# Kernel optimization log

Hardware: AMD Instinct MI355X
Metric: run time of the kernel (lower is better)

The kernel has to match this reference:

```python
import jax, jax.numpy as jnp
import numpy as np

N_NODES = 50000
N_EDGES = 600000
D_IN, D_HID, D_OUT = 128, 128, 64
KEEP_PROB = 0.5  # TF2: dp = args.dropout used as rate; kept mask values clip to 1.0


def setup_inputs() -> dict:
    key = jax.random.key(0)
    k = jax.random.split(key, 6)
    x = jax.random.normal(k[0], (N_NODES, D_IN), dtype=jnp.float32)
    edge_row = jax.random.randint(k[1], (N_EDGES,), 0, N_NODES, dtype=jnp.int64)
    edge_col = jax.random.randint(k[2], (N_EDGES,), 0, N_NODES, dtype=jnp.int64)
    edge_vals = jnp.ones((N_EDGES,), dtype=jnp.float32)
    # tf.nn.dropout(ones)->clip(max=1)->bool is a Bernoulli(keep) edge mask
    edge_mask = jax.random.bernoulli(k[3], KEEP_PROB, (N_EDGES,))
    W0 = jax.random.normal(k[4], (D_IN, D_HID), dtype=jnp.float32) * 0.05
    W1 = jax.random.normal(k[5], (D_HID, D_OUT), dtype=jnp.float32) * 0.05
    return {"x": x, "edge_row": edge_row, "edge_col": edge_col,
            "edge_vals": edge_vals, "edge_mask": edge_mask, "W0": W0, "W1": W1}


def reference(x, edge_row, edge_col, edge_vals, edge_mask, W0, W1):
    N = x.shape[0]
    # drop edges by zeroing values (equivalent to boolean_mask compaction)
    ev = edge_vals * edge_mask.astype(edge_vals.dtype)
    loop = jnp.arange(N, dtype=edge_row.dtype)
    row = jnp.concatenate([edge_row, loop])            # + sparse identity
    col = jnp.concatenate([edge_col, loop])
    vals = jnp.concatenate([ev, jnp.ones((N,), ev.dtype)])
    # degree renormalization: D^{-1/2} (A+I) D^{-1/2}
    deg = jax.ops.segment_sum(vals, row, num_segments=N)
    d_inv_sqrt = jnp.clip(deg ** -0.5, 0.0, 10.0)
    nvals = vals * d_inv_sqrt[row] * d_inv_sqrt[col]

    def spmm(h):  # support @ h via gather-multiply-scatter
        return jax.ops.segment_sum(nvals[:, None] * h[col], row, num_segments=N)

    h = jax.nn.relu(spmm(x @ W0))
    out = spmm(h @ W1)  # last layer: identity activation
    return out
```

## Files before the change

### kernel.cpp

```cpp
#include <hip/hip_runtime.h>
#include <hip/hip_bf16.h>


#define BLK 256
#define PADW 32

typedef __attribute__((ext_vector_type(8))) short short8v;
typedef __attribute__((ext_vector_type(8))) unsigned short ushort8v;
typedef __attribute__((ext_vector_type(4))) unsigned short ushort4v;
typedef __attribute__((ext_vector_type(4))) float float4v;

__device__ inline unsigned short f2b(float f) {
    __hip_bfloat16 h = __float2bfloat16(f);
    return *reinterpret_cast<unsigned short*>(&h);
}
__device__ inline float b2f(unsigned short u) {
    unsigned int v = (unsigned int)u << 16;
    return *reinterpret_cast<float*>(&v);
}

__global__ __launch_bounds__(BLK) void prepK(const float* __restrict__ W0,
                                             const float* __restrict__ W1,
                                             unsigned short* __restrict__ W0T,
                                             unsigned short* __restrict__ W1T,
                                             int* __restrict__ counts, int n) {
    int i = blockIdx.x * BLK + threadIdx.x;
    if (i < n) counts[i] = 0;
    if (i < 128 * 128) {
        int c = i >> 7, k = i & 127;
        W0T[i] = f2b(W0[k * 128 + c]);
    } else if (i < 128 * 128 + 64 * 128) {
        int j = i - 128 * 128;
        int c = j >> 7, k = j & 127;
        W1T[j] = f2b(W1[k * 64 + c]);
    }
}

__global__ __launch_bounds__(BLK) void phase1K(const int* __restrict__ erow,
                                               const int* __restrict__ ecolin,
                                               const int* __restrict__ emask,
                                               int* __restrict__ counts,
                                               int* __restrict__ epack, int e,
                                               const float* __restrict__ X,
                                               const unsigned short* __restrict__ W0T,
                                               unsigned short* __restrict__ XW,
                                               int M, int nbE) {
    constexpr int NC = 128, NT = NC / 16;
    __shared__ __align__(16) unsigned short sB[NC * 128];
    int t = threadIdx.x;

    if ((int)blockIdx.x < nbE) {
        int base = blockIdx.x * (2 * BLK) + t;
#pragma unroll
        for (int u = 0; u < 2; u++) {
            int i = base + u * BLK;
            if (i < e && emask[i]) {
                int r = erow[i];
                int rank = atomicAdd(&counts[r], 1);
                if (rank < PADW) epack[(size_t)r * PADW + rank] = ecolin[i];
            }
        }
        return;
    }

    int row0 = (blockIdx.x - nbE) * 64;
    for (int ch = t; ch < NC * 16; ch += BLK) {
        int row = ch >> 4, c16 = ch & 15;
        int dst = row * 128 + ((c16 * 8) ^ ((row & 7) << 3));
        *(ushort8v*)&sB[dst] = *(const ushort8v*)&W0T[row * 128 + c16 * 8];
    }
    __syncthreads();

    int w = t >> 6, l = t & 63;
    int arow = row0 + w * 16 + (l & 15);
    int kgrp = l >> 4;
    int bcol = l & 15;
    bool aval = arow < M;
    const float* Arow = X + (size_t)(aval ? arow : 0) * 128;

    float4v acc[NT];
#pragma unroll
    for (int nt = 0; nt < NT; nt++) acc[nt] = {0.f, 0.f, 0.f, 0.f};
#pragma unroll
    for (int ks = 0; ks < 4; ks++) {
        int koff = ks * 32 + kgrp * 8;
        float4 a0 = make_float4(0.f, 0.f, 0.f, 0.f);
        float4 a1 = make_float4(0.f, 0.f, 0.f, 0.f);
        if (aval) {
            a0 = *(const float4*)&Arow[koff];
            a1 = *(const float4*)&Arow[koff + 4];
        }
        short8v av;
        av[0] = (short)f2b(a0.x); av[1] = (short)f2b(a0.y);
        av[2] = (short)f2b(a0.z); av[3] = (short)f2b(a0.w);
        av[4] = (short)f2b(a1.x); av[5] = (short)f2b(a1.y);
        av[6] = (short)f2b(a1.z); av[7] = (short)f2b(a1.w);
#pragma unroll
        for (int nt = 0; nt < NT; nt++) {
            int brow = nt * 16 + bcol;
            short8v bv = *(short8v*)&sB[brow * 128 + (koff ^ ((brow & 7) << 3))];
            acc[nt] = __builtin_amdgcn_mfma_f32_16x16x32_bf16(av, bv, acc[nt], 0, 0, 0);
        }
    }
    int crow0 = row0 + w * 16 + kgrp * 4;
#pragma unroll
    for (int nt = 0; nt < NT; nt++) {
#pragma unroll
        for (int j = 0; j < 4; j++) {
            int r = crow0 + j;
            if (r < M) XW[(size_t)r * NC + nt * 16 + bcol] = f2b(acc[nt][j]);
        }
    }
}

__global__ __launch_bounds__(BLK) void fuse1K(const unsigned short* __restrict__ XW,
                                              const int* __restrict__ counts,
                                              const int* __restrict__ epack,
                                              const unsigned short* __restrict__ W1T,
                                              unsigned short* __restrict__ HW1s, int n) {
    __shared__ __align__(16) unsigned short sA[32 * 128];
    __shared__ __align__(16) int2 sE[32 * PADW];
    __shared__ int sK[32];
    __shared__ float sD[32];
    int t = threadIdx.x;
    int row0 = blockIdx.x * 32;

    {
        const int* esrc = epack + (size_t)row0 * PADW;
        for (int q = t; q < 32 * PADW; q += BLK) {
            int c = esrc[q];
            c = ((unsigned)c < (unsigned)n) ? c : 0;
            float dc = fminf(rsqrtf(1.0f + (float)counts[c]), 10.0f);
            sE[q] = make_int2(c, __float_as_int(dc));
        }
    }
    if (t < 32) {
        int r = row0 + t;
        int cnt = (r < n) ? counts[r] : 0;
        sK[t] = min(cnt, PADW);
        sD[t] = (r < n) ? fminf(rsqrtf(1.0f + (float)cnt), 10.0f) : 0.f;
    }
    __syncthreads();

    int g = t >> 3, li = t & 7;
    int d0 = li * 16;
    {
        int lr = g;
        int r = row0 + lr;
        int k = sK[lr];
        float dis = sD[lr];
        float acc[16];
        if (r < n) {
            ushort8v s0 = *(const ushort8v*)&XW[(size_t)r * 128 + d0];
            ushort8v s1 = *(const ushort8v*)&XW[(size_t)r * 128 + d0 + 8];
#pragma unroll
            for (int q = 0; q < 8; q++) {
                acc[q] = dis * b2f(s0[q]);
                acc[8 + q] = dis * b2f(s1[q]);
            }
        } else {
#pragma unroll
            for (int q = 0; q < 16; q++) acc[q] = 0.f;
        }
        const int2* eL = &sE[lr * PADW];
        for (int i = 0; i < k; i += 4) {
            int i1 = i + 1 < k ? i + 1 : k - 1;
            int i2 = i + 2 < k ? i + 2 : k - 1;
            int i3 = i + 3 < k ? i + 3 : k - 1;
            int2 e0 = eL[i], e1 = eL[i1], e2 = eL[i2], e3 = eL[i3];
            float v0 = __int_as_float(e0.y);
            float v1 = (i + 1 < k) ? __int_as_float(e1.y) : 0.f;
            float v2 = (i + 2 < k) ? __int_as_float(e2.y) : 0.f;
            float v3 = (i + 3 < k) ? __int_as_float(e3.y) : 0.f;
            ushort8v ga0 = *(const ushort8v*)&XW[(size_t)e0.x * 128 + d0];
            ushort8v gb0 = *(const ushort8v*)&XW[(size_t)e0.x * 128 + d0 + 8];
            ushort8v ga1 = *(const ushort8v*)&XW[(size_t)e1.x * 128 + d0];
            ushort8v gb1 = *(const ushort8v*)&XW[(size_t)e1.x * 128 + d0 + 8];
            ushort8v ga2 = *(const ushort8v*)&XW[(size_t)e2.x * 128 + d0];
            ushort8v gb2 = *(const ushort8v*)&XW[(size_t)e2.x * 128 + d0 + 8];
            ushort8v ga3 = *(const ushort8v*)&XW[(size_t)e3.x * 128 + d0];
            ushort8v gb3 = *(const ushort8v*)&XW[(size_t)e3.x * 128 + d0 + 8];
#pragma unroll
            for (int q = 0; q < 8; q++) {
                acc[q]     += v0 * b2f(ga0[q]) + v1 * b2f(ga1[q])
                            + v2 * b2f(ga2[q]) + v3 * b2f(ga3[q]);
                acc[8 + q] += v0 * b2f(gb0[q]) + v1 * b2f(gb1[q])
                            + v2 * b2f(gb2[q]) + v3 * b2f(gb3[q]);
            }
        }
        ushort8v h0, h1;
#pragma unroll
        for (int q = 0; q < 8; q++) {
            h0[q] = f2b(fmaxf(acc[q], 0.f) * dis);
            h1[q] = f2b(fmaxf(acc[8 + q], 0.f) * dis);
        }
        int sw = (lr & 7) << 3;
        *(ushort8v*)&sA[lr * 128 + (d0 ^ sw)] = h0;
        *(ushort8v*)&sA[lr * 128 + ((d0 + 8) ^ sw)] = h1;
    }
    __syncthreads();

    int w = t >> 6, l = t & 63;
    int rt = w & 1, ct = w >> 1;
    int arow = rt * 16 + (l & 15);
    int kgrp = l >> 4;
    int bcol = l & 15;
    float4v acc2[2];
    acc2[0] = {0.f, 0.f, 0.f, 0.f};
    acc2[1] = {0.f, 0.f, 0.f, 0.f};
#pragma unroll
    for (int ks = 0; ks < 4; ks++) {
        int koff = ks * 32 + kgrp * 8;
        short8v av = *(short8v*)&sA[arow * 128 + (koff ^ ((arow & 7) << 3))];
#pragma unroll
        for (int nt = 0; nt < 2; nt++) {
            int brow = ct * 32 + nt * 16 + bcol;
            short8v bv = *(const short8v*)&W1T[brow * 128 + koff];
            acc2[nt] = __builtin_amdgcn_mfma_f32_16x16x32_bf16(av, bv, acc2[nt], 0, 0, 0);
        }
    }
    int lrow0 = rt * 16 + kgrp * 4;
#pragma unroll
    for (int nt = 0; nt < 2; nt++) {
#pragma unroll
        for (int j = 0; j < 4; j++) {
            int r = row0 + lrow0 + j;
            if (r < n)
                HW1s[(size_t)r * 64 + ct * 32 + nt * 16 + bcol] =
                    f2b(acc2[nt][j] * sD[lrow0 + j]);
        }
    }
}

__global__ __launch_bounds__(BLK) void spmm2K(const unsigned short* __restrict__ HW1s,
                                              const int* __restrict__ counts,
                                              const int* __restrict__ epack,
                                              float* __restrict__ out, int n) {
    int t = threadIdx.x;
    int r = blockIdx.x * 32 + (t >> 3);
    int li = t & 7;
    if (r >= n) return;
    int cnt = counts[r];
    int k = min(cnt, PADW);
    int d0 = li * 8;
    float acc[8];
    {
        ushort8v sv = *(const ushort8v*)&HW1s[(size_t)r * 64 + d0];
#pragma unroll
        for (int q = 0; q < 8; q++) acc[q] = b2f(sv[q]);
    }
    const int* eb = epack + (size_t)r * PADW;
    for (int i = 0; i < k; i += 8) {
        int cc[8];
        float vv[8];
#pragma unroll
        for (int j = 0; j < 8; j++) {
            int idx = (i + j < k) ? i + j : k - 1;
            cc[j] = eb[idx];
            vv[j] = (i + j < k) ? 1.f : 0.f;
        }
        ushort8v gg[8];
#pragma unroll
        for (int j = 0; j < 8; j++)
            gg[j] = *(const ushort8v*)&HW1s[(size_t)cc[j] * 64 + d0];
#pragma unroll
        for (int j = 0; j < 8; j++) {
#pragma unroll
            for (int q = 0; q < 8; q++) acc[q] += vv[j] * b2f(gg[j][q]);
        }
    }
    float dis = fminf(rsqrtf(1.0f + (float)cnt), 10.0f);
    float4 o0 = make_float4(acc[0] * dis, acc[1] * dis, acc[2] * dis, acc[3] * dis);
    float4 o1 = make_float4(acc[4] * dis, acc[5] * dis, acc[6] * dis, acc[7] * dis);
    *(float4*)&out[(size_t)r * 64 + d0] = o0;
    *(float4*)&out[(size_t)r * 64 + d0 + 4] = o1;
}


extern "C" void kernel_launch(void* const* d_in, const int* in_sizes, int n_in,
                              void* d_out, int out_size, void* d_ws, size_t ws_size,
                              hipStream_t stream) {
    const float* x = (const float*)d_in[0];
    const int* erow = (const int*)d_in[1];
    const int* ecolin = (const int*)d_in[2];
    const int* emask = (const int*)d_in[4];
    const float* W0 = (const float*)d_in[5];
    const float* W1 = (const float*)d_in[6];
    float* out = (float*)d_out;

    const int n = in_sizes[0] / 128;
    const int e = in_sizes[1];

    char* ws = (char*)d_ws;
    size_t off = 0;
    auto alloc = [&](size_t bytes) {
        void* p = ws + off;
        off += (bytes + 255) & ~(size_t)255;
        return p;
    };
    int* counts = (int*)alloc((size_t)n * 4);
    int* epack = (int*)alloc((size_t)n * PADW * 4);
    unsigned short* W0T = (unsigned short*)alloc(128 * 128 * 2);
    unsigned short* W1T = (unsigned short*)alloc(64 * 128 * 2);
    unsigned short* XW = (unsigned short*)alloc((size_t)n * 128 * 2);
    unsigned short* HW1s = (unsigned short*)alloc((size_t)n * 64 * 2);

    int nbP = (n + BLK - 1) / BLK;
    int nbE = (e + 2 * BLK - 1) / (2 * BLK);
    int nbG = (n + 63) / 64;
    int nbF = (n + 31) / 32;
    int nbS = (n + 31) / 32;

    prepK<<<nbP, BLK, 0, stream>>>(W0, W1, W0T, W1T, counts, n);
    phase1K<<<nbE + nbG, BLK, 0, stream>>>(erow, ecolin, emask,
                                           counts, epack, e,
                                           x, W0T, XW, n, nbE);
    fuse1K<<<nbF, BLK, 0, stream>>>(XW, counts, epack, W1T, HW1s, n);
    spmm2K<<<nbS, BLK, 0, stream>>>(HW1s, counts, epack, out, n);
}
```

Before: 69.39 us.

## Fold weight prep into phase1 kernel and replace count zeroing with memset

Removes the separate prep kernel. Each GEMM block now converts and transposes W0 from fp32 directly into shared memory, W1 transposition runs in extra tail blocks of phase1, and the counts buffer is cleared with hipMemsetAsync. GEMM blocks now process two 64-row tiles each so the per-block W0 staging is amortized, and edge blocks handle four edges per thread. The aim is to drop one kernel launch and its serialization. The cost is redundant W0 conversion in every GEMM block, scalar strided shared-memory stores, and fewer blocks for the GEMM.

```diff
diff --git a/kernel.cpp b/kernel.cpp
--- a/kernel.cpp
+++ b/kernel.cpp
@@ -17,23 +17,6 @@
 __device__ inline float b2f(unsigned short u) {
     unsigned int v = (unsigned int)u << 16;
     return *reinterpret_cast<float*>(&v);
-}
-
-__global__ __launch_bounds__(BLK) void prepK(const float* __restrict__ W0,
-                                             const float* __restrict__ W1,
-                                             unsigned short* __restrict__ W0T,
-                                             unsigned short* __restrict__ W1T,
-                                             int* __restrict__ counts, int n) {
-    int i = blockIdx.x * BLK + threadIdx.x;
-    if (i < n) counts[i] = 0;
-    if (i < 128 * 128) {
-        int c = i >> 7, k = i & 127;
-        W0T[i] = f2b(W0[k * 128 + c]);
-    } else if (i < 128 * 128 + 64 * 128) {
-        int j = i - 128 * 128;
-        int c = j >> 7, k = j & 127;
-        W1T[j] = f2b(W1[k * 64 + c]);
-    }
 }
 
 __global__ __launch_bounds__(BLK) void phase1K(const int* __restrict__ erow,
@@ -42,17 +25,20 @@
                                                int* __restrict__ counts,
                                                int* __restrict__ epack, int e,
                                                const float* __restrict__ X,
-                                               const unsigned short* __restrict__ W0T,
+                                               const float* __restrict__ W0,
+                                               const float* __restrict__ W1,
+                                               unsigned short* __restrict__ W1T,
                                                unsigned short* __restrict__ XW,
-                                               int M, int nbE) {
+                                               int M, int nbE, int nbG) {
     constexpr int NC = 128, NT = NC / 16;
     __shared__ __align__(16) unsigned short sB[NC * 128];
     int t = threadIdx.x;
-
-    if ((int)blockIdx.x < nbE) {
-        int base = blockIdx.x * (2 * BLK) + t;
-#pragma unroll
-        for (int u = 0; u < 2; u++) {
+    int bid = blockIdx.x;
+
+    if (bid < nbE) {
+        int base = bid * (4 * BLK) + t;
+#pragma unroll
+        for (int u = 0; u < 4; u++) {
             int i = base + u * BLK;
             if (i < e && emask[i]) {
                 int r = erow[i];
@@ -62,53 +48,67 @@
         }
         return;
     }
-
-    int row0 = (blockIdx.x - nbE) * 64;
-    for (int ch = t; ch < NC * 16; ch += BLK) {
-        int row = ch >> 4, c16 = ch & 15;
-        int dst = row * 128 + ((c16 * 8) ^ ((row & 7) << 3));
-        *(ushort8v*)&sB[dst] = *(const ushort8v*)&W0T[row * 128 + c16 * 8];
+    if (bid >= nbE + nbG) {
+        int idx = (bid - nbE - nbG) * BLK + t;
+        if (idx < 64 * 128) {
+            int c = idx >> 7, k = idx & 127;
+            W1T[idx] = f2b(W1[k * 64 + c]);
+        }
+        return;
+    }
+
+    for (int q = t; q < 128 * 32; q += BLK) {
+        int k = q >> 5, c4 = (q & 31) << 2;
+        float4 v = *(const float4*)&W0[k * 128 + c4];
+        sB[(c4 + 0) * 128 + (k ^ (((c4 + 0) & 7) << 3))] = f2b(v.x);
+        sB[(c4 + 1) * 128 + (k ^ (((c4 + 1) & 7) << 3))] = f2b(v.y);
+        sB[(c4 + 2) * 128 + (k ^ (((c4 + 2) & 7) << 3))] = f2b(v.z);
+        sB[(c4 + 3) * 128 + (k ^ (((c4 + 3) & 7) << 3))] = f2b(v.w);
     }
     __syncthreads();
 
     int w = t >> 6, l = t & 63;
-    int arow = row0 + w * 16 + (l & 15);
     int kgrp = l >> 4;
     int bcol = l & 15;
-    bool aval = arow < M;
-    const float* Arow = X + (size_t)(aval ? arow : 0) * 128;
-
-    float4v acc[NT];
-#pragma unroll
-    for (int nt = 0; nt < NT; nt++) acc[nt] = {0.f, 0.f, 0.f, 0.f};
-#pragma unroll
-    for (int ks = 0; ks < 4; ks++) {
-        int koff = ks * 32 + kgrp * 8;
-        float4 a0 = make_float4(0.f, 0.f, 0.f, 0.f);
-        float4 a1 = make_float4(0.f, 0.f, 0.f, 0.f);
-        if (aval) {
-            a0 = *(const float4*)&Arow[koff];
-            a1 = *(const float4*)&Arow[koff + 4];
-        }
-        short8v av;
-        av[0] = (short)f2b(a0.x); av[1] = (short)f2b(a0.y);
-        av[2] = (short)f2b(a0.z); av[3] = (short)f2b(a0.w);
-        av[4] = (short)f2b(a1.x); av[5] = (short)f2b(a1.y);
-        av[6] = (short)f2b(a1.z); av[7] = (short)f2b(a1.w);
+#pragma unroll
+    for (int rtile = 0; rtile < 2; rtile++) {
+        int row0 = (bid - nbE) * 128 + rtile * 64;
+        int arow = row0 + w * 16 + (l & 15);
+        bool aval = arow < M;
+        const float* Arow = X + (size_t)(aval ? arow : 0) * 128;
+
+        float4v acc[NT];
+#pragma unroll
+        for (int nt = 0; nt < NT; nt++) acc[nt] = {0.f, 0.f, 0.f, 0.f};
+#pragma unroll
+        for (int ks = 0; ks < 4; ks++) {
+            int koff = ks * 32 + kgrp * 8;
+            float4 a0 = make_float4(0.f, 0.f, 0.f, 0.f);
+            float4 a1 = make_float4(0.f, 0.f, 0.f, 0.f);
+            if (aval) {
+                a0 = *(const float4*)&Arow[koff];
+                a1 = *(const float4*)&Arow[koff + 4];
+            }
+            short8v av;
+            av[0] = (short)f2b(a0.x); av[1] = (short)f2b(a0.y);
+            av[2] = (short)f2b(a0.z); av[3] = (short)f2b(a0.w);
+            av[4] = (short)f2b(a1.x); av[5] = (short)f2b(a1.y);
+            av[6] = (short)f2b(a1.z); av[7] = (short)f2b(a1.w);
+#pragma unroll
+            for (int nt = 0; nt < NT; nt++) {
+                int brow = nt * 16 + bcol;
+                short8v bv = *(short8v*)&sB[brow * 128 + (koff ^ ((brow & 7) << 3))];
+                acc[nt] = __builtin_amdgcn_mfma_f32_16x16x32_bf16(av, bv, acc[nt], 0, 0, 0);
+            }
+        }
+        int crow0 = row0 + w * 16 + kgrp * 4;
 #pragma unroll
         for (int nt = 0; nt < NT; nt++) {
-            int brow = nt * 16 + bcol;
-            short8v bv = *(short8v*)&sB[brow * 128 + (koff ^ ((brow & 7) << 3))];
-            acc[nt] = __builtin_amdgcn_mfma_f32_16x16x32_bf16(av, bv, acc[nt], 0, 0, 0);
-        }
-    }
-    int crow0 = row0 + w * 16 + kgrp * 4;
-#pragma unroll
-    for (int nt = 0; nt < NT; nt++) {
-#pragma unroll
-        for (int j = 0; j < 4; j++) {
-            int r = crow0 + j;
-            if (r < M) XW[(size_t)r * NC + nt * 16 + bcol] = f2b(acc[nt][j]);
+#pragma unroll
+            for (int j = 0; j < 4; j++) {
+                int r = crow0 + j;
+                if (r < M) XW[(size_t)r * NC + nt * 16 + bcol] = f2b(acc[nt][j]);
+            }
         }
     }
 }
@@ -300,21 +300,20 @@
     };
     int* counts = (int*)alloc((size_t)n * 4);
     int* epack = (int*)alloc((size_t)n * PADW * 4);
-    unsigned short* W0T = (unsigned short*)alloc(128 * 128 * 2);
     unsigned short* W1T = (unsigned short*)alloc(64 * 128 * 2);
     unsigned short* XW = (unsigned short*)alloc((size_t)n * 128 * 2);
     unsigned short* HW1s = (unsigned short*)alloc((size_t)n * 64 * 2);
 
-    int nbP = (n + BLK - 1) / BLK;
-    int nbE = (e + 2 * BLK - 1) / (2 * BLK);
-    int nbG = (n + 63) / 64;
+    int nbE = (e + 4 * BLK - 1) / (4 * BLK);
+    int nbG = (n + 127) / 128;
+    int nbT = (64 * 128 + BLK - 1) / BLK;
     int nbF = (n + 31) / 32;
     int nbS = (n + 31) / 32;
 
-    prepK<<<nbP, BLK, 0, stream>>>(W0, W1, W0T, W1T, counts, n);
-    phase1K<<<nbE + nbG, BLK, 0, stream>>>(erow, ecolin, emask,
-                                           counts, epack, e,
-                                           x, W0T, XW, n, nbE);
+    hipMemsetAsync(counts, 0, (size_t)n * 4, stream);
+    phase1K<<<nbE + nbG + nbT, BLK, 0, stream>>>(erow, ecolin, emask,
+                                                 counts, epack, e,
+                                                 x, W0, W1, W1T, XW, n, nbE, nbG);
     fuse1K<<<nbF, BLK, 0, stream>>>(XW, counts, epack, W1T, HW1s, n);
     spmm2K<<<nbS, BLK, 0, stream>>>(HW1s, counts, epack, out, n);
 }
```

New measurement: 74.64 us. +7.6%, slower.
